# Kernel optimization log

Hardware: AMD Instinct MI355X
Metric: run time of the kernel (lower is better)

The kernel has to match this reference:

```python
import jax, jax.numpy as jnp
import numpy as np

SCALE = 1.0 / np.sqrt(64.0)  # hard-coded 64**0.5 in original, independent of dims


def setup_inputs() -> dict:
    key = jax.random.key(0)
    k1, k2 = jax.random.split(key)
    x = jax.random.normal(k1, (8, 2048, 1024), dtype=jnp.float32)
    # kernel[0]=W_Q, kernel[1]=W_K, kernel[2]=W_V, each [d_in, d_out]
    kernel = jax.random.normal(k2, (3, 1024, 1024), dtype=jnp.float32) * 0.02
    return {"x": x, "kernel": kernel}


def reference(x, kernel):
    # x: [b, s, d_in], kernel: [3, d_in, d_out]
    wq = jnp.einsum('bsd,de->bse', x, kernel[0])
    wk = jnp.einsum('bsd,de->bse', x, kernel[1])
    wv = jnp.einsum('bsd,de->bse', x, kernel[2])
    scores = jnp.einsum('bqe,bke->bqk', wq, wk) * SCALE  # [b, s, s]
    attn = jax.nn.softmax(scores, axis=-1)
    return jnp.einsum('bqk,bke->bqe', attn, wv)  # [b, s, d_out]
```

## Files before the change

### kernel.cpp

```cpp
#include <hip/hip_runtime.h>
#include <stdint.h>

typedef unsigned short u16;
typedef unsigned short u16x8 __attribute__((ext_vector_type(8)));
typedef _Float16 f16x8 __attribute__((ext_vector_type(8)));
typedef float f32x4 __attribute__((ext_vector_type(4)));

__device__ __forceinline__ u16 f2h(float f) {
  _Float16 x = (_Float16)f;
  return __builtin_bit_cast(u16, x);
}
__device__ __forceinline__ float h2f(u16 h) {
  _Float16 x = __builtin_bit_cast(_Float16, h);
  return (float)x;
}

__device__ __forceinline__ void gld16(const void* g, void* l) {
  __builtin_amdgcn_global_load_lds(
      (const __attribute__((address_space(1))) unsigned int*)g,
      (__attribute__((address_space(3))) unsigned int*)l,
      16, 0, 0);
}

#define TBM 256
#define TBN 256
#define TBK 64

template <int QM, int QN>
__device__ __forceinline__ void mfma_quad(f32x4 (&acc)[8][4],
                                          const f16x8 (&ar)[4][2],
                                          const f16x8 (&br)[2][2]) {
#pragma unroll
  for (int mm = 0; mm < 4; ++mm)
#pragma unroll
    for (int nn = 0; nn < 2; ++nn)
#pragma unroll
      for (int kk = 0; kk < 2; ++kk)
        acc[QM * 4 + mm][QN * 2 + nn] = __builtin_amdgcn_mfma_f32_16x16x32_f16(
            ar[mm][kk], br[nn][kk], acc[QM * 4 + mm][QN * 2 + nn], 0, 0, 0);
}

template <int OUT>
__global__ __launch_bounds__(512, 2) void gemm256(
    const u16* __restrict__ Ap, const u16* __restrict__ Bp,
    void* __restrict__ Cp, int K, int lda, int ldb, int ldc,
    long sA, long sB, long sC) {
  __shared__ char lds[131072];

  const int gx = gridDim.x, gy = gridDim.y;
  const int lin = (blockIdx.z * gy + blockIdx.y) * gx + blockIdx.x;
  const int cpx = (gx * gy * gridDim.z) >> 3;
  const int swz = (lin & 7) * cpx + (lin >> 3);
  const int bx = swz % gx;
  const int tq = swz / gx;
  const int by = tq % gy;
  const int z = tq / gy;

  const int tid = threadIdx.x;
  const int lane = tid & 63, wid = tid >> 6;
  const int wr = wid >> 2, wc = wid & 3;
  const int l15 = lane & 15, l4 = lane >> 4;
  const int bm = by * TBM, bn = bx * TBN;

  const u16* Ag = Ap + (long)z * sA + (long)bm * lda;
  const u16* Bg = Bp + (long)z * sB + (long)bn * ldb;
  const u16* Ah[2] = {Ag, Ag + 128L * lda};
  const u16* Bh[2] = {Bg, Bg + 128L * ldb};

  auto stageHalf = [&](const u16* gbase, int ld, int buf, int which, int k0) {
#pragma unroll
    for (int it = 0; it < 2; ++it) {
      int idx = it * 512 + tid;
      int r = idx >> 3, p = idx & 7;
      int s = p ^ (r & 7);
      gld16(gbase + (long)r * ld + k0 + s * 8,
            lds + buf * 65536 + which * 16384 + (it * 512 + wid * 64) * 16);
    }
  };

  auto dsA = [&](int buf, int qm, f16x8 (&ar)[4][2]) {
#pragma unroll
    for (int mm = 0; mm < 4; ++mm)
#pragma unroll
      for (int kk = 0; kk < 2; ++kk) {
        int lr = qm * 64 + mm * 16 + l15;
        int slot = kk * 4 + l4;
        ar[mm][kk] = *(const f16x8*)(lds + buf * 65536 + wr * 16384 +
                                     lr * 128 + ((slot ^ (lr & 7)) * 16));
      }
  };
  auto dsB = [&](int buf, int qn, f16x8 (&br)[2][2]) {
#pragma unroll
    for (int nn = 0; nn < 2; ++nn)
#pragma unroll
      for (int kk = 0; kk < 2; ++kk) {
        int lr = (wc & 1) * 64 + (qn * 2 + nn) * 16 + l15;
        int slot = kk * 4 + l4;
        br[nn][kk] = *(const f16x8*)(lds + buf * 65536 +
                                     (2 + (wc >> 1)) * 16384 + lr * 128 +
                                     ((slot ^ (lr & 7)) * 16));
      }
  };

  f32x4 acc[8][4] = {};
  const int nk = K / TBK;

  stageHalf(Ah[0], lda, 0, 0, 0);
  stageHalf(Ah[1], lda, 0, 1, 0);
  stageHalf(Bh[0], ldb, 0, 2, 0);
  stageHalf(Bh[1], ldb, 0, 3, 0);
  if (nk > 1) {
    stageHalf(Ah[0], lda, 1, 0, TBK);
    stageHalf(Ah[1], lda, 1, 1, TBK);
    asm volatile("s_waitcnt vmcnt(4)" ::: "memory");
  } else {
    asm volatile("s_waitcnt vmcnt(0)" ::: "memory");
  }
  __builtin_amdgcn_s_barrier();
  __builtin_amdgcn_sched_barrier(0);

  for (int t = 0; t < nk; ++t) {
    const int buf = t & 1;
    f16x8 a0[4][2], a1[4][2], b0[2][2], b1[2][2];

    dsA(buf, 0, a0);
    dsB(buf, 0, b0);
    if (t + 1 < nk) stageHalf(Bh[0], ldb, buf ^ 1, 2, (t + 1) * TBK);
    __builtin_amdgcn_s_barrier();
    asm volatile("s_waitcnt lgkmcnt(0)" ::: "memory");
    __builtin_amdgcn_sched_barrier(0);
    __builtin_amdgcn_s_setprio(1);
    mfma_quad<0, 0>(acc, a0, b0);
    __builtin_amdgcn_s_setprio(0);
    __builtin_amdgcn_sched_barrier(0);
    __builtin_amdgcn_s_barrier();

    dsA(buf, 1, a1);
    if (t + 1 < nk) stageHalf(Bh[1], ldb, buf ^ 1, 3, (t + 1) * TBK);
    __builtin_amdgcn_s_barrier();
    asm volatile("s_waitcnt lgkmcnt(0)" ::: "memory");
    __builtin_amdgcn_sched_barrier(0);
    __builtin_amdgcn_s_setprio(1);
    mfma_quad<1, 0>(acc, a1, b0);
    __builtin_amdgcn_s_setprio(0);
    __builtin_amdgcn_sched_barrier(0);
    __builtin_amdgcn_s_barrier();

    dsB(buf, 1, b1);
    if (t + 2 < nk) stageHalf(Ah[0], lda, buf, 0, (t + 2) * TBK);
    __builtin_amdgcn_s_barrier();
    asm volatile("s_waitcnt lgkmcnt(0)" ::: "memory");
    __builtin_amdgcn_sched_barrier(0);
    __builtin_amdgcn_s_setprio(1);
    mfma_quad<0, 1>(acc, a0, b1);
    __builtin_amdgcn_s_setprio(0);
    __builtin_amdgcn_sched_barrier(0);
    __builtin_amdgcn_s_barrier();

    if (t + 2 < nk) {
      stageHalf(Ah[1], lda, buf, 1, (t + 2) * TBK);
      asm volatile("s_waitcnt vmcnt(4)" ::: "memory");
    } else if (t + 1 < nk) {
      asm volatile("s_waitcnt vmcnt(0)" ::: "memory");
    }
    __builtin_amdgcn_s_barrier();
    __builtin_amdgcn_sched_barrier(0);
    __builtin_amdgcn_s_setprio(1);
    mfma_quad<1, 1>(acc, a1, b1);
    __builtin_amdgcn_s_setprio(0);
    __builtin_amdgcn_sched_barrier(0);
    __builtin_amdgcn_s_barrier();
  }

  if constexpr (OUT == 1) {
    u16* C = (u16*)Cp + (long)z * sC;
#pragma unroll
    for (int m = 0; m < 8; ++m)
#pragma unroll
      for (int n = 0; n < 4; ++n) {
        int row = bm + wr * 128 + m * 16 + l4 * 4;
        int col = bn + wc * 64 + n * 16 + l15;
#pragma unroll
        for (int r = 0; r < 4; ++r)
          C[(long)(row + r) * ldc + col] = f2h(acc[m][n][r]);
      }
  } else {
    float* C = (float*)Cp + (long)z * sC;
#pragma unroll
    for (int m = 0; m < 8; ++m)
#pragma unroll
      for (int n = 0; n < 4; ++n) {
        int row = bm + wr * 128 + m * 16 + l4 * 4;
        int col = bn + wc * 64 + n * 16 + l15;
#pragma unroll
        for (int r = 0; r < 4; ++r)
          C[(long)(row + r) * ldc + col] = acc[m][n][r];
      }
  }
}

template <typename TIN>
__global__ __launch_bounds__(256) void transpose_to_f16(
    const TIN* __restrict__ in, u16* __restrict__ out, int R, int C, int ldin,
    long sIn, long sOut) {
  __shared__ u16 T[64][72];
  const long bi = blockIdx.z;
  const TIN* ip = in + bi * sIn;
  u16* op = out + bi * sOut;
  const int r0 = blockIdx.y * 64, c0 = blockIdx.x * 64;
  const int t = threadIdx.x, c8 = t & 7, rr = t >> 3;
#pragma unroll
  for (int h = 0; h < 2; ++h) {
    const int r = rr + h * 32;
    u16x8 v;
    if constexpr (sizeof(TIN) == 4) {
      const float* g = (const float*)ip + (long)(r0 + r) * ldin + c0 + c8 * 8;
      float4 a = *(const float4*)g;
      float4 b = *(const float4*)(g + 4);
      v[0] = f2h(a.x); v[1] = f2h(a.y); v[2] = f2h(a.z); v[3] = f2h(a.w);
      v[4] = f2h(b.x); v[5] = f2h(b.y); v[6] = f2h(b.z); v[7] = f2h(b.w);
    } else {
      v = *(const u16x8*)((const u16*)ip + (long)(r0 + r) * ldin + c0 + c8 * 8);
    }
    *(u16x8*)&T[r][c8 * 8] = v;
  }
  __syncthreads();
#pragma unroll
  for (int h = 0; h < 2; ++h) {
    const int oc = rr + h * 32;
    u16x8 v;
#pragma unroll
    for (int j = 0; j < 8; ++j) v[j] = T[c8 * 8 + j][oc];
    *(u16x8*)(op + (long)(c0 + oc) * R + r0 + c8 * 8) = v;
  }
}

__global__ __launch_bounds__(256) void f32_to_f16(const float* __restrict__ in,
                                                  u16* __restrict__ out,
                                                  long n8) {
  long i = (long)blockIdx.x * 256 + threadIdx.x;
  const long stride = (long)gridDim.x * 256;
  for (; i < n8; i += stride) {
    const float* g = in + i * 8;
    float4 a = *(const float4*)g;
    float4 b = *(const float4*)(g + 4);
    u16x8 o;
    o[0] = f2h(a.x); o[1] = f2h(a.y); o[2] = f2h(a.z); o[3] = f2h(a.w);
    o[4] = f2h(b.x); o[5] = f2h(b.y); o[6] = f2h(b.z); o[7] = f2h(b.w);
    *(u16x8*)(out + i * 8) = o;
  }
}

__global__ __launch_bounds__(256) void softmax_rows(u16* __restrict__ S) {
  const long row = blockIdx.x;
  u16* p = S + row * 2048;
  const int tid = threadIdx.x, lane = tid & 63, wid = tid >> 6;
  u16x8 v = *(const u16x8*)(p + tid * 8);
  float x[8];
#pragma unroll
  for (int j = 0; j < 8; ++j) x[j] = h2f(v[j]);
  float m = x[0];
#pragma unroll
  for (int j = 1; j < 8; ++j) m = fmaxf(m, x[j]);
#pragma unroll
  for (int d = 1; d < 64; d <<= 1) m = fmaxf(m, __shfl_xor(m, d, 64));
  __shared__ float rmax[4], rsum[4];
  if (lane == 0) rmax[wid] = m;
  __syncthreads();
  m = fmaxf(fmaxf(rmax[0], rmax[1]), fmaxf(rmax[2], rmax[3]));
  float e[8];
  float s = 0.f;
#pragma unroll
  for (int j = 0; j < 8; ++j) {
    e[j] = __expf((x[j] - m) * 0.125f);
    s += e[j];
  }
#pragma unroll
  for (int d = 1; d < 64; d <<= 1) s += __shfl_xor(s, d, 64);
  if (lane == 0) rsum[wid] = s;
  __syncthreads();
  s = rsum[0] + rsum[1] + rsum[2] + rsum[3];
  const float inv = 1.0f / s;
  u16x8 o;
#pragma unroll
  for (int j = 0; j < 8; ++j) o[j] = f2h(e[j] * inv);
  *(u16x8*)(p + tid * 8) = o;
}

extern "C" void kernel_launch(void* const* d_in, const int* in_sizes, int n_in,
                              void* d_out, int out_size, void* d_ws,
                              size_t ws_size, hipStream_t stream) {
  const float* x = (const float*)d_in[0];
  const float* w = (const float*)d_in[1];
  float* out = (float*)d_out;

  u16* ws = (u16*)d_ws;
  u16* QKV = ws;
  u16* Wt = ws + 50331648L;
  u16* Vt = ws + 53477376L;
  u16* xh = ws + 70254592L;
  u16* S = ws + 70254592L;

  f32_to_f16<<<2048, 256, 0, stream>>>(x, xh, 2097152L);

  transpose_to_f16<float><<<dim3(16, 16, 3), 256, 0, stream>>>(
      w, Wt, 1024, 1024, 1024, 1048576L, 1048576L);

  gemm256<1><<<dim3(12, 64, 1), 512, 0, stream>>>(
      xh, Wt, (void*)QKV, 1024, 1024, 1024, 3072, 0L, 0L, 0L);

  transpose_to_f16<u16><<<dim3(16, 32, 8), 256, 0, stream>>>(
      QKV + 2048, Vt, 2048, 1024, 3072, 6291456L, 2097152L);

  gemm256<1><<<dim3(8, 8, 8), 512, 0, stream>>>(
      QKV, QKV + 1024, (void*)S, 1024, 3072, 3072, 2048, 6291456L, 6291456L,
      4194304L);

  softmax_rows<<<dim3(16384), 256, 0, stream>>>(S);

  gemm256<0><<<dim3(4, 8, 8), 512, 0, stream>>>(
      S, Vt, (void*)out, 2048, 2048, 2048, 1024, 4194304L, 2097152L,
      2097152L);
}
```

Measured before the change: 309.6 us.

## Software-pipeline LDS fragment loads one phase ahead of MFMA quads

Issues each LDS-to-register fragment load one phase before the MFMA quad that uses it, and prefetches the next iteration's first A/B fragments during the last quad. This hides LDS read latency behind matrix math instead of waiting on lgkmcnt before every quad. Explicit waits and scheduling barriers are replaced by compiler memory fences, so the compiler must insert waits itself. This gives it more freedom to reorder, at the cost of higher register pressure and possible ordering hazards.

```diff
diff --git a/kernel.cpp b/kernel.cpp
--- a/kernel.cpp
+++ b/kernel.cpp
@@ -21,6 +21,8 @@
       (__attribute__((address_space(3))) unsigned int*)l,
       16, 0, 0);
 }
+
+#define MEMFENCE asm volatile("" ::: "memory")
 
 #define TBM 256
 #define TBN 256
@@ -103,59 +105,58 @@
   };
 
   f32x4 acc[8][4] = {};
+  f16x8 a0[4][2], a1[4][2], b0[2][2], b1[2][2];
   const int nk = K / TBK;
 
   stageHalf(Ah[0], lda, 0, 0, 0);
   stageHalf(Ah[1], lda, 0, 1, 0);
   stageHalf(Bh[0], ldb, 0, 2, 0);
   stageHalf(Bh[1], ldb, 0, 3, 0);
-  if (nk > 1) {
-    stageHalf(Ah[0], lda, 1, 0, TBK);
-    stageHalf(Ah[1], lda, 1, 1, TBK);
-    asm volatile("s_waitcnt vmcnt(4)" ::: "memory");
-  } else {
-    asm volatile("s_waitcnt vmcnt(0)" ::: "memory");
-  }
+  stageHalf(Ah[0], lda, 1, 0, TBK);
+  stageHalf(Ah[1], lda, 1, 1, TBK);
+  asm volatile("s_waitcnt vmcnt(4)" ::: "memory");
   __builtin_amdgcn_s_barrier();
-  __builtin_amdgcn_sched_barrier(0);
+  MEMFENCE;
+  dsA(0, 0, a0);
+  dsB(0, 0, b0);
 
   for (int t = 0; t < nk; ++t) {
     const int buf = t & 1;
-    f16x8 a0[4][2], a1[4][2], b0[2][2], b1[2][2];
-
-    dsA(buf, 0, a0);
-    dsB(buf, 0, b0);
+
+    dsA(buf, 1, a1);
     if (t + 1 < nk) stageHalf(Bh[0], ldb, buf ^ 1, 2, (t + 1) * TBK);
-    __builtin_amdgcn_s_barrier();
-    asm volatile("s_waitcnt lgkmcnt(0)" ::: "memory");
-    __builtin_amdgcn_sched_barrier(0);
+    MEMFENCE;
+    __builtin_amdgcn_s_barrier();
+    MEMFENCE;
     __builtin_amdgcn_s_setprio(1);
     mfma_quad<0, 0>(acc, a0, b0);
     __builtin_amdgcn_s_setprio(0);
-    __builtin_amdgcn_sched_barrier(0);
-    __builtin_amdgcn_s_barrier();
-
-    dsA(buf, 1, a1);
+    MEMFENCE;
+    __builtin_amdgcn_s_barrier();
+    MEMFENCE;
+
+    dsB(buf, 1, b1);
     if (t + 1 < nk) stageHalf(Bh[1], ldb, buf ^ 1, 3, (t + 1) * TBK);
-    __builtin_amdgcn_s_barrier();
-    asm volatile("s_waitcnt lgkmcnt(0)" ::: "memory");
-    __builtin_amdgcn_sched_barrier(0);
+    MEMFENCE;
+    __builtin_amdgcn_s_barrier();
+    MEMFENCE;
     __builtin_amdgcn_s_setprio(1);
     mfma_quad<1, 0>(acc, a1, b0);
     __builtin_amdgcn_s_setprio(0);
-    __builtin_amdgcn_sched_barrier(0);
-    __builtin_amdgcn_s_barrier();
-
-    dsB(buf, 1, b1);
+    MEMFENCE;
+    __builtin_amdgcn_s_barrier();
+    MEMFENCE;
+
     if (t + 2 < nk) stageHalf(Ah[0], lda, buf, 0, (t + 2) * TBK);
-    __builtin_amdgcn_s_barrier();
-    asm volatile("s_waitcnt lgkmcnt(0)" ::: "memory");
-    __builtin_amdgcn_sched_barrier(0);
+    MEMFENCE;
+    __builtin_amdgcn_s_barrier();
+    MEMFENCE;
     __builtin_amdgcn_s_setprio(1);
     mfma_quad<0, 1>(acc, a0, b1);
     __builtin_amdgcn_s_setprio(0);
-    __builtin_amdgcn_sched_barrier(0);
-    __builtin_amdgcn_s_barrier();
+    MEMFENCE;
+    __builtin_amdgcn_s_barrier();
+    MEMFENCE;
 
     if (t + 2 < nk) {
       stageHalf(Ah[1], lda, buf, 1, (t + 2) * TBK);
@@ -164,12 +165,17 @@
       asm volatile("s_waitcnt vmcnt(0)" ::: "memory");
     }
     __builtin_amdgcn_s_barrier();
-    __builtin_amdgcn_sched_barrier(0);
+    MEMFENCE;
+    if (t + 1 < nk) {
+      dsA(buf ^ 1, 0, a0);
+      dsB(buf ^ 1, 0, b0);
+    }
     __builtin_amdgcn_s_setprio(1);
     mfma_quad<1, 1>(acc, a1, b1);
     __builtin_amdgcn_s_setprio(0);
-    __builtin_amdgcn_sched_barrier(0);
-    __builtin_amdgcn_s_barrier();
+    MEMFENCE;
+    __builtin_amdgcn_s_barrier();
+    MEMFENCE;
   }
 
   if constexpr (OUT == 1) {
```

After: 308.5 us. About the same (-0.4%).

## Deepen GEMM prefetch pipeline and precompute LDS/global addresses

Applied to the files above, without the earlier changes.

Restructures the 256x256 GEMM main loop. Address offsets for the LDS reads and global-to-LDS loads are precomputed per thread, and the loop is unrolled by two so the buffer index is a compile-time constant. The prefetch schedule is shifted so three quarter-tiles are in flight (vmcnt 6 instead of 4), with a partial lgkmcnt wait before the first barrier. The MFMA order is also changed to kk-outer. The goal is less address arithmetic and more overlap of loads with MFMA, at the cost of tighter waitcnt reasoning and an implicit assumption that nk is even.

```diff
diff --git a/kernel.cpp b/kernel.cpp
--- a/kernel.cpp
+++ b/kernel.cpp
@@ -22,6 +22,17 @@
       16, 0, 0);
 }
 
+#define BAR __builtin_amdgcn_s_barrier()
+#define SCHEDB __builtin_amdgcn_sched_barrier(0)
+#define LGKM0                                        \
+  do {                                               \
+    asm volatile("s_waitcnt lgkmcnt(0)" ::: "memory"); \
+    __builtin_amdgcn_sched_barrier(0);               \
+  } while (0)
+#define LGKM8 asm volatile("s_waitcnt lgkmcnt(8)" ::: "memory")
+#define VM6 asm volatile("s_waitcnt vmcnt(6)" ::: "memory")
+#define VM0 asm volatile("s_waitcnt vmcnt(0)" ::: "memory")
+
 #define TBM 256
 #define TBN 256
 #define TBK 64
@@ -31,11 +42,11 @@
                                           const f16x8 (&ar)[4][2],
                                           const f16x8 (&br)[2][2]) {
 #pragma unroll
-  for (int mm = 0; mm < 4; ++mm)
-#pragma unroll
-    for (int nn = 0; nn < 2; ++nn)
-#pragma unroll
-      for (int kk = 0; kk < 2; ++kk)
+  for (int kk = 0; kk < 2; ++kk)
+#pragma unroll
+    for (int mm = 0; mm < 4; ++mm)
+#pragma unroll
+      for (int nn = 0; nn < 2; ++nn)
         acc[QM * 4 + mm][QN * 2 + nn] = __builtin_amdgcn_mfma_f32_16x16x32_f16(
             ar[mm][kk], br[nn][kk], acc[QM * 4 + mm][QN * 2 + nn], 0, 0, 0);
 }
@@ -64,112 +75,124 @@
 
   const u16* Ag = Ap + (long)z * sA + (long)bm * lda;
   const u16* Bg = Bp + (long)z * sB + (long)bn * ldb;
-  const u16* Ah[2] = {Ag, Ag + 128L * lda};
-  const u16* Bh[2] = {Bg, Bg + 128L * ldb};
-
-  auto stageHalf = [&](const u16* gbase, int ld, int buf, int which, int k0) {
-#pragma unroll
-    for (int it = 0; it < 2; ++it) {
-      int idx = it * 512 + tid;
-      int r = idx >> 3, p = idx & 7;
-      int s = p ^ (r & 7);
-      gld16(gbase + (long)r * ld + k0 + s * 8,
-            lds + buf * 65536 + which * 16384 + (it * 512 + wid * 64) * 16);
-    }
-  };
-
-  auto dsA = [&](int buf, int qm, f16x8 (&ar)[4][2]) {
-#pragma unroll
-    for (int mm = 0; mm < 4; ++mm)
-#pragma unroll
-      for (int kk = 0; kk < 2; ++kk) {
-        int lr = qm * 64 + mm * 16 + l15;
-        int slot = kk * 4 + l4;
-        ar[mm][kk] = *(const f16x8*)(lds + buf * 65536 + wr * 16384 +
-                                     lr * 128 + ((slot ^ (lr & 7)) * 16));
+
+  const int sw = l15 & 7;
+  const int s0 = (l4 ^ sw) * 16, s1 = ((4 + l4) ^ sw) * 16;
+  int aB[2][2], bB[2][2];
+  aB[0][0] = wr * 16384 + l15 * 128 + s0;
+  aB[0][1] = wr * 16384 + l15 * 128 + s1;
+  bB[0][0] = 32768 + (wc >> 1) * 16384 + ((wc & 1) * 64 + l15) * 128 + s0;
+  bB[0][1] = 32768 + (wc >> 1) * 16384 + ((wc & 1) * 64 + l15) * 128 + s1;
+  aB[1][0] = aB[0][0] + 65536;
+  aB[1][1] = aB[0][1] + 65536;
+  bB[1][0] = bB[0][0] + 65536;
+  bB[1][1] = bB[0][1] + 65536;
+
+#define DSA(BUF, QM, AR)                                                     \
+  do {                                                                       \
+    _Pragma("unroll") for (int mm = 0; mm < 4; ++mm) {                       \
+      AR[mm][0] = *(const f16x8*)(lds + aB[BUF][0] + (QM)*8192 + mm * 2048); \
+      AR[mm][1] = *(const f16x8*)(lds + aB[BUF][1] + (QM)*8192 + mm * 2048); \
+    }                                                                        \
+  } while (0)
+#define DSB(BUF, QN, BR)                                                     \
+  do {                                                                       \
+    _Pragma("unroll") for (int nn = 0; nn < 2; ++nn) {                       \
+      BR[nn][0] = *(const f16x8*)(lds + bB[BUF][0] + (QN)*4096 + nn * 2048); \
+      BR[nn][1] = *(const f16x8*)(lds + bB[BUF][1] + (QN)*4096 + nn * 2048); \
+    }                                                                        \
+  } while (0)
+
+  const u16 *gpA0[2], *gpA1[2], *gpB0[2], *gpB1[2];
+  int loA0[2], loA1[2], loB0[2], loB1[2];
+  {
+    const u16* bases[4] = {Ag, Ag + 128L * lda, Bg, Bg + 128L * ldb};
+    const int lds_[4] = {lda, lda, ldb, ldb};
+    const u16** gps[4] = {gpA0, gpA1, gpB0, gpB1};
+    int* los[4] = {loA0, loA1, loB0, loB1};
+#pragma unroll
+    for (int X = 0; X < 4; ++X)
+#pragma unroll
+      for (int it = 0; it < 2; ++it) {
+        int idx = it * 512 + tid, r = idx >> 3, p = idx & 7, s = p ^ (r & 7);
+        gps[X][it] = bases[X] + (long)r * lds_[X] + s * 8;
+        los[X][it] = X * 16384 + (it * 512 + wid * 64) * 16;
       }
-  };
-  auto dsB = [&](int buf, int qn, f16x8 (&br)[2][2]) {
-#pragma unroll
-    for (int nn = 0; nn < 2; ++nn)
-#pragma unroll
-      for (int kk = 0; kk < 2; ++kk) {
-        int lr = (wc & 1) * 64 + (qn * 2 + nn) * 16 + l15;
-        int slot = kk * 4 + l4;
-        br[nn][kk] = *(const f16x8*)(lds + buf * 65536 +
-                                     (2 + (wc >> 1)) * 16384 + lr * 128 +
-                                     ((slot ^ (lr & 7)) * 16));
-      }
-  };
+  }
+#define STAGE(X, BUF, kt)                                            \
+  do {                                                               \
+    long ko = (long)(kt) << 7;                                       \
+    gld16((const char*)gp##X[0] + ko, lds + ((BUF)*65536 + lo##X[0])); \
+    gld16((const char*)gp##X[1] + ko, lds + ((BUF)*65536 + lo##X[1])); \
+  } while (0)
 
   f32x4 acc[8][4] = {};
+  f16x8 a0[4][2], a1[4][2], b0[2][2], b1[2][2];
   const int nk = K / TBK;
 
-  stageHalf(Ah[0], lda, 0, 0, 0);
-  stageHalf(Ah[1], lda, 0, 1, 0);
-  stageHalf(Bh[0], ldb, 0, 2, 0);
-  stageHalf(Bh[1], ldb, 0, 3, 0);
-  if (nk > 1) {
-    stageHalf(Ah[0], lda, 1, 0, TBK);
-    stageHalf(Ah[1], lda, 1, 1, TBK);
-    asm volatile("s_waitcnt vmcnt(4)" ::: "memory");
-  } else {
-    asm volatile("s_waitcnt vmcnt(0)" ::: "memory");
-  }
-  __builtin_amdgcn_s_barrier();
-  __builtin_amdgcn_sched_barrier(0);
-
-  for (int t = 0; t < nk; ++t) {
-    const int buf = t & 1;
-    f16x8 a0[4][2], a1[4][2], b0[2][2], b1[2][2];
-
-    dsA(buf, 0, a0);
-    dsB(buf, 0, b0);
-    if (t + 1 < nk) stageHalf(Bh[0], ldb, buf ^ 1, 2, (t + 1) * TBK);
-    __builtin_amdgcn_s_barrier();
-    asm volatile("s_waitcnt lgkmcnt(0)" ::: "memory");
-    __builtin_amdgcn_sched_barrier(0);
-    __builtin_amdgcn_s_setprio(1);
-    mfma_quad<0, 0>(acc, a0, b0);
-    __builtin_amdgcn_s_setprio(0);
-    __builtin_amdgcn_sched_barrier(0);
-    __builtin_amdgcn_s_barrier();
-
-    dsA(buf, 1, a1);
-    if (t + 1 < nk) stageHalf(Bh[1], ldb, buf ^ 1, 3, (t + 1) * TBK);
-    __builtin_amdgcn_s_barrier();
-    asm volatile("s_waitcnt lgkmcnt(0)" ::: "memory");
-    __builtin_amdgcn_sched_barrier(0);
-    __builtin_amdgcn_s_setprio(1);
-    mfma_quad<1, 0>(acc, a1, b0);
-    __builtin_amdgcn_s_setprio(0);
-    __builtin_amdgcn_sched_barrier(0);
-    __builtin_amdgcn_s_barrier();
-
-    dsB(buf, 1, b1);
-    if (t + 2 < nk) stageHalf(Ah[0], lda, buf, 0, (t + 2) * TBK);
-    __builtin_amdgcn_s_barrier();
-    asm volatile("s_waitcnt lgkmcnt(0)" ::: "memory");
-    __builtin_amdgcn_sched_barrier(0);
-    __builtin_amdgcn_s_setprio(1);
-    mfma_quad<0, 1>(acc, a0, b1);
-    __builtin_amdgcn_s_setprio(0);
-    __builtin_amdgcn_sched_barrier(0);
-    __builtin_amdgcn_s_barrier();
-
-    if (t + 2 < nk) {
-      stageHalf(Ah[1], lda, buf, 1, (t + 2) * TBK);
-      asm volatile("s_waitcnt vmcnt(4)" ::: "memory");
-    } else if (t + 1 < nk) {
-      asm volatile("s_waitcnt vmcnt(0)" ::: "memory");
-    }
-    __builtin_amdgcn_s_barrier();
-    __builtin_amdgcn_sched_barrier(0);
-    __builtin_amdgcn_s_setprio(1);
-    mfma_quad<1, 1>(acc, a1, b1);
-    __builtin_amdgcn_s_setprio(0);
-    __builtin_amdgcn_sched_barrier(0);
-    __builtin_amdgcn_s_barrier();
+  STAGE(A0, 0, 0);
+  STAGE(A1, 0, 0);
+  STAGE(B0, 0, 0);
+  STAGE(B1, 0, 0);
+  STAGE(A0, 1, 1);
+  STAGE(A1, 1, 1);
+  STAGE(B0, 1, 1);
+  VM6;
+  BAR;
+  SCHEDB;
+
+#define TILE(BUF, t)                                              \
+  do {                                                            \
+                    \
+    DSA(BUF, 0, a0);                                              \
+    DSB(BUF, 0, b0);                                              \
+    if ((t) + 1 < nk) STAGE(B1, BUF ^ 1, (t) + 1);                \
+    LGKM8;                                                        \
+    BAR;                                                          \
+    LGKM0;                                                        \
+    __builtin_amdgcn_s_setprio(1);                                \
+    mfma_quad<0, 0>(acc, a0, b0);                                 \
+    __builtin_amdgcn_s_setprio(0);                                \
+    SCHEDB;                                                       \
+    BAR;                                                          \
+                        \
+    DSA(BUF, 1, a1);                                              \
+    if ((t) + 2 < nk) STAGE(A0, BUF, (t) + 2);                    \
+    BAR;                                                          \
+    LGKM0;                                                        \
+    __builtin_amdgcn_s_setprio(1);                                \
+    mfma_quad<1, 0>(acc, a1, b0);                                 \
+    __builtin_amdgcn_s_setprio(0);                                \
+    SCHEDB;                                                       \
+    BAR;                                                          \
+                        \
+    DSB(BUF, 1, b1);                                              \
+    if ((t) + 2 < nk) STAGE(A1, BUF, (t) + 2);                    \
+    BAR;                                                          \
+    LGKM0;                                                        \
+    __builtin_amdgcn_s_setprio(1);                                \
+    mfma_quad<0, 1>(acc, a0, b1);                                 \
+    __builtin_amdgcn_s_setprio(0);                                \
+    SCHEDB;                                                       \
+    BAR;                                                          \
+     \
+    if ((t) + 2 < nk) {                                           \
+      STAGE(B0, BUF, (t) + 2);                                    \
+      VM6;                                                        \
+    } else if ((t) + 1 < nk) {                                    \
+      VM0;                                                        \
+    }                                                             \
+    BAR;                                                          \
+    __builtin_amdgcn_s_setprio(1);                                \
+    mfma_quad<1, 1>(acc, a1, b1);                                 \
+    __builtin_amdgcn_s_setprio(0);                                \
+    SCHEDB;                                                       \
+    BAR;                                                          \
+  } while (0)
+
+  for (int t = 0; t < nk; t += 2) {
+    TILE(0, t);
+    TILE(1, t + 1);
   }
 
   if constexpr (OUT == 1) {
@@ -197,6 +220,10 @@
           C[(long)(row + r) * ldc + col] = acc[m][n][r];
       }
   }
+#undef TILE
+#undef STAGE
+#undef DSA
+#undef DSB
 }
 
 template <typename TIN>
```

After: 304.7 us. Within noise of the previous version (-1.6%).
